# Kernel optimization log

Measured on AMD Instinct MI355X. Metric: run time of the kernel, lower is better.

## Reference

```python
import jax, jax.numpy as jnp
import numpy as np

# Static problem sizes (match input_specs): B graphs of NPG nodes each.
B = 64        # number of graphs in the batch
NPG = 1024    # nodes per graph
N = B * NPG   # total nodes
F = 64        # node feature dim
H = 128       # MLP hidden/output dim
K = 16        # knn neighbors (loop=False)


def setup_inputs() -> dict:
    key = jax.random.key(0)
    k1, k2, k3 = jax.random.split(key, 3)
    x = jax.random.normal(k1, (N, F), dtype=jnp.float32)
    batch = jnp.repeat(jnp.arange(B, dtype=jnp.int32), NPG)  # sorted graph ids
    W1 = jax.random.normal(k2, (2 * F, H), dtype=jnp.float32) / np.float32(np.sqrt(2 * F))
    b1 = jnp.zeros((H,), dtype=jnp.float32)
    W2 = jax.random.normal(k3, (H, H), dtype=jnp.float32) / np.float32(np.sqrt(H))
    b2 = jnp.zeros((H,), dtype=jnp.float32)
    return {"x": x, "batch": batch, "W1": W1, "b1": b1, "W2": W2, "b2": b2}


def _knn_edge_index(x):
    """PyG-style knn_graph (flow='source_to_target', loop=False) per graph.
    Returns (row, col) = edge_index[0], edge_index[1] where row = neighbor
    (source) node, col = center (target) node; each center has exactly K edges.
    Assumes batch ids are contiguous blocks of NPG nodes (as in setup_inputs)."""
    xb = x.reshape(B, NPG, F)
    sq = jnp.sum(xb * xb, axis=-1)                                   # [B, n]
    d = sq[:, :, None] + sq[:, None, :] - 2.0 * jnp.einsum('bnf,bmf->bnm', xb, xb)
    d = d + jnp.eye(NPG, dtype=d.dtype) * jnp.float32(1e10)          # no self loops
    _, nbr = jax.lax.top_k(-d, K)                                    # [B, n, K] local neighbor ids
    offs = (jnp.arange(B, dtype=jnp.int32) * NPG)[:, None, None]
    row = (nbr.astype(jnp.int32) + offs).reshape(-1)                 # neighbors (edge_index[0])
    centers = jnp.arange(N, dtype=jnp.int32).reshape(B, NPG, 1)
    col = jnp.broadcast_to(centers, (B, NPG, K)).reshape(-1)         # centers  (edge_index[1])
    return row, col


def reference(x, batch, W1, b1, W2, b2):
    # edge_index = knn_graph(x, k, batch, loop=False); row, col = edge_index
    row, col = _knn_edge_index(x)
    x_center = x[row]                                   # [E, F] gather
    x_neighbor = x[col]                                 # [E, F] gather
    ef = jnp.concatenate([x_center, x_neighbor - x_center], axis=-1)  # [E, 2F]
    # nn_module: Linear -> ReLU -> Linear -> ReLU
    h = jax.nn.relu(ef @ W1 + b1)
    h = jax.nn.relu(h @ W2 + b2)                        # [E, H]
    # manual scatter-mean onto row (index_add + bincount.clamp(min=1))
    node_features = jax.ops.segment_sum(h, row, num_segments=N)
    counts = jax.ops.segment_sum(jnp.ones((row.shape[0],), dtype=x.dtype), row, num_segments=N)
    counts = jnp.maximum(counts, 1.0)
    return node_features / counts[:, None]
```

## Files before the change

### kernel.cpp

```cpp
#include <hip/hip_runtime.h>

typedef __attribute__((ext_vector_type(4))) float f32x4;
typedef __attribute__((ext_vector_type(4))) unsigned int u32x4;
typedef __attribute__((ext_vector_type(8))) short s16x8;
typedef __attribute__((ext_vector_type(8))) _Float16 f16x8;

#define N_NODES 65536
#define GNPG 1024
#define FDIM 64
#define HDIM 128
#define KNN 16
#define JT 64
#define DSTR 68
#define SCAND 20
#define STKC 6
#define NEDGE (N_NODES * KNN)
#define NT (NEDGE / 64)

__global__ void prep_node_k(const float* __restrict__ x, float* __restrict__ sq,
                            double* __restrict__ sq64, _Float16* __restrict__ xf,
                            const float* __restrict__ W2, _Float16* __restrict__ w2f,
                            const float* __restrict__ W1, _Float16* __restrict__ w1cf) {
  if (blockIdx.x >= 1024) {
    int tid = threadIdx.x;
    if (blockIdx.x == 1024) {
      for (int idx = tid; idx < 8 * 4 * 64 * 8; idx += 256) {
        int j = idx & 7, l = (idx >> 3) & 63, ks = (idx >> 9) & 3, ct = idx >> 11;
        int k = 8 * (l >> 4) + j + 32 * ks, col = ct * 16 + (l & 15);
        w2f[idx] = (_Float16)W2[k * 128 + col];
      }
    } else {
      for (int idx = tid; idx < 16 * 2 * 64 * 8; idx += 256) {
        int j = idx & 7, l = (idx >> 3) & 63, ks = (idx >> 9) & 1, ct = idx >> 10;
        int k = 8 * (l >> 4) + j + 32 * ks, col = ct * 16 + (l & 15);
        float v = (col < 128) ? (W1[k * 128 + col] - W1[(k + 64) * 128 + col])
                              : W1[(k + 64) * 128 + (col - 128)];
        w1cf[idx] = (_Float16)v;
      }
    }
    return;
  }
  int t = blockIdx.x * 256 + threadIdx.x;
  int n = t >> 2, q = t & 3;
  const f32x4* xp = (const f32x4*)(x + (size_t)n * FDIM + q * 16);
  double s = 0;
  f16x8 h0, h1;
#pragma unroll
  for (int c8 = 0; c8 < 2; ++c8) {
    f32x4 a = xp[2 * c8], b = xp[2 * c8 + 1];
    f16x8 h;
#pragma unroll
    for (int e = 0; e < 4; ++e) {
      h[e] = (_Float16)a[e];
      h[4 + e] = (_Float16)b[e];
      s = fma((double)a[e], (double)a[e], s);
      s = fma((double)b[e], (double)b[e], s);
    }
    if (c8 == 0) h0 = h; else h1 = h;
  }
  *(f16x8*)(xf + (size_t)n * FDIM + q * 16) = h0;
  *(f16x8*)(xf + (size_t)n * FDIM + q * 16 + 8) = h1;
  s += __shfl_xor(s, 1);
  s += __shfl_xor(s, 2);
  if (q == 0) { sq64[n] = s; sq[n] = (float)s; }
}

__global__ __launch_bounds__(256) void prep_pq_k(const _Float16* __restrict__ xf,
                                                 const _Float16* __restrict__ w1cf,
                                                 const float* __restrict__ b1,
                                                 _Float16* __restrict__ PQ16) {
  __shared__ __attribute__((aligned(16))) _Float16 wcL[16384];
  int tid = threadIdx.x, lane = tid & 63, wave = tid >> 6;
  for (int i = tid; i < 2048; i += 256)
    *(f16x8*)(wcL + i * 8) = *(const f16x8*)(w1cf + i * 8);
  int rbase = blockIdx.x * 128 + wave * 32;
  f16x8 af[2][2];
#pragma unroll
  for (int rt = 0; rt < 2; ++rt)
#pragma unroll
    for (int ks = 0; ks < 2; ++ks) {
      size_t off = (size_t)(rbase + rt * 16 + (lane & 15)) * FDIM + (lane >> 4) * 8 + 32 * ks;
      af[rt][ks] = *(const f16x8*)(xf + off);
    }
  __syncthreads();
  f32x4 acc[2][16];
#pragma unroll
  for (int rt = 0; rt < 2; ++rt)
#pragma unroll
    for (int ct = 0; ct < 16; ++ct) acc[rt][ct] = (f32x4){0.f, 0.f, 0.f, 0.f};
#pragma unroll
  for (int ks = 0; ks < 2; ++ks)
#pragma unroll
    for (int ct = 0; ct < 16; ++ct) {
      f16x8 b = *(const f16x8*)(wcL + ((ct * 2 + ks) * 64 + lane) * 8);
#pragma unroll
      for (int rt = 0; rt < 2; ++rt)
        acc[rt][ct] = __builtin_amdgcn_mfma_f32_16x16x32_f16(af[rt][ks], b, acc[rt][ct], 0, 0, 0);
    }
  float b1r[16];
#pragma unroll
  for (int ct = 0; ct < 16; ++ct)
    b1r[ct] = (ct >= 8) ? b1[(ct - 8) * 16 + (lane & 15)] : 0.f;
#pragma unroll
  for (int rt = 0; rt < 2; ++rt)
#pragma unroll
    for (int ct = 0; ct < 16; ++ct) {
      int col = ct * 16 + (lane & 15);
#pragma unroll
      for (int r = 0; r < 4; ++r) {
        int row = rbase + rt * 16 + (lane >> 4) * 4 + r;
        PQ16[(size_t)row * 256 + col] = (_Float16)(acc[rt][ct][r] + b1r[ct]);
      }
    }
}

__global__ __launch_bounds__(256) void knn1_k(const _Float16* __restrict__ xf,
                                              const float* __restrict__ sq,
                                              unsigned short* __restrict__ candi) {
  __shared__ float sq_l[GNPG];
  __shared__ __attribute__((aligned(16))) _Float16 bfL[512 * 8];
  __shared__ __attribute__((aligned(16))) unsigned keyL[128 * DSTR];
  __shared__ __attribute__((aligned(16))) unsigned stk[STKC * 256];
  int tid = threadIdx.x, lane = tid & 63, wave = tid >> 6;
  int g = blockIdx.x >> 3;
  int rb = (blockIdx.x & 7) * 128;
  const _Float16* xfg = xf + (size_t)g * GNPG * FDIM;
  for (int i = tid; i < GNPG; i += 256) sq_l[i] = sq[g * GNPG + i] + 0.5f;
  f16x8 af[2][2];
#pragma unroll
  for (int rt = 0; rt < 2; ++rt)
#pragma unroll
    for (int ks = 0; ks < 2; ++ks) {
      size_t off = (size_t)(rb + wave * 32 + rt * 16 + (lane & 15)) * FDIM + (lane >> 4) * 8 + 32 * ks;
      af[rt][ks] = *(const f16x8*)(xfg + off);
    }
  unsigned dl[SCAND];
#pragma unroll
  for (int q = 0; q < SCAND; ++q) dl[q] = 0xFFFFFFFFu;
  int c = tid >> 1, sub = tid & 1;
  int sp = 0;
  for (int jt = 0; jt < GNPG / JT; ++jt) {
#pragma unroll
    for (int s2 = tid; s2 < 512; s2 += 256) {
      int ct = s2 >> 7, ks = (s2 >> 6) & 1, l = s2 & 63;
      size_t goff = (size_t)(jt * JT + ct * 16 + (l & 15)) * FDIM + (l >> 4) * 8 + 32 * ks;
      *(f16x8*)(bfL + s2 * 8) = *(const f16x8*)(xfg + goff);
    }
    __syncthreads();
    f32x4 acc[2][4];
#pragma unroll
    for (int rt = 0; rt < 2; ++rt)
#pragma unroll
      for (int ct = 0; ct < 4; ++ct) acc[rt][ct] = (f32x4){0.f, 0.f, 0.f, 0.f};
#pragma unroll
    for (int ks = 0; ks < 2; ++ks)
#pragma unroll
      for (int ct = 0; ct < 4; ++ct) {
        f16x8 bfr = *(const f16x8*)(bfL + ((ct * 2 + ks) * 64 + lane) * 8);
#pragma unroll
        for (int rt = 0; rt < 2; ++rt)
          acc[rt][ct] = __builtin_amdgcn_mfma_f32_16x16x32_f16(af[rt][ks], bfr, acc[rt][ct], 0, 0, 0);
      }
#pragma unroll
    for (int rt = 0; rt < 2; ++rt)
#pragma unroll
      for (int ct = 0; ct < 4; ++ct) {
        int coltl = ct * 16 + (lane & 15);
        int jlg = jt * JT + coltl;
        float sqj = sq_l[jlg];
#pragma unroll
        for (int r = 0; r < 4; ++r) {
          int row = wave * 32 + rt * 16 + (lane >> 4) * 4 + r;
          float d = sq_l[rb + row] + sqj - 2.f * acc[rt][ct][r];
          unsigned key = (__float_as_uint(d) & 0xFFFFFC00u) | (unsigned)jlg;
          if (rb + row == jlg) key = 0xFFFFFFFFu;
          keyL[row * DSTR + coltl] = key;
        }
      }
    __syncthreads();
    const unsigned* kp = keyL + c * DSTR + sub * 32;
#pragma unroll 2
    for (int i = 0; i < 8; ++i) {
      if (__any(sp > STKC - 4)) {
        while (__any(sp > 0)) {
          if (sp > 0) {
            --sp;
            unsigned k = stk[sp * 256 + tid];
            if (k < dl[SCAND - 1]) {
              dl[SCAND - 1] = k;
#pragma unroll
              for (int p = SCAND - 1; p >= 1; --p) {
                unsigned mn = min(dl[p - 1], dl[p]);
                unsigned mx = max(dl[p - 1], dl[p]);
                dl[p - 1] = mn; dl[p] = mx;
              }
            }
          }
        }
      }
      u32x4 v = *(const u32x4*)(kp + i * 4);
#pragma unroll
      for (int e = 0; e < 4; ++e) {
        stk[sp * 256 + tid] = v[e];
        sp += (v[e] < dl[SCAND - 1]) ? 1 : 0;
      }
    }
  }
  while (__any(sp > 0)) {
    if (sp > 0) {
      --sp;
      unsigned k = stk[sp * 256 + tid];
      if (k < dl[SCAND - 1]) {
        dl[SCAND - 1] = k;
#pragma unroll
        for (int p = SCAND - 1; p >= 1; --p) {
          unsigned mn = min(dl[p - 1], dl[p]);
          unsigned mx = max(dl[p - 1], dl[p]);
          dl[p - 1] = mn; dl[p] = mx;
        }
      }
    }
  }
  int nglob = g * GNPG + rb + c;
  unsigned short* ii = candi + (size_t)nglob * (2 * SCAND) + sub * SCAND;
#pragma unroll
  for (int q = 0; q < SCAND; ++q) ii[q] = (unsigned short)(dl[q] & 1023u);
}

__global__ __launch_bounds__(256) void knn2_k(const float* __restrict__ x,
                                              const double* __restrict__ sq64,
                                              const unsigned short* __restrict__ candi,
                                              int* __restrict__ nbr, int* __restrict__ counts) {
  __shared__ double md[2][128][17];
  __shared__ unsigned short mi[2][128][17];
  int tid = threadIdx.x, c_local = tid >> 1, sub = tid & 1;
  int n = blockIdx.x * 128 + c_local;
  int gbase = n & ~(GNPG - 1);
  f32x4 xi[16];
  const f32x4* xp = (const f32x4*)(x + (size_t)n * FDIM);
#pragma unroll
  for (int f = 0; f < 16; ++f) xi[f] = xp[f];
  double sq64i = sq64[n];
  double dl[KNN]; int il[KNN];
#pragma unroll
  for (int q = 0; q < KNN; ++q) { dl[q] = 1.0e300; il[q] = 0x7FFFFFFF; }
  const unsigned short* ii = candi + (size_t)n * (2 * SCAND) + sub * SCAND;
#pragma unroll 1
  for (int t = 0; t < SCAND; ++t) {
    int jl = ii[t];
    int j = gbase + jl;
    const f32x4* xj = (const f32x4*)(x + (size_t)j * FDIM);
    double t0 = 0, t1 = 0, t2 = 0, t3 = 0;
#pragma unroll
    for (int f = 0; f < 16; ++f) {
      f32x4 a = xi[f], b = xj[f];
      t0 = fma((double)a[0], (double)b[0], t0);
      t1 = fma((double)a[1], (double)b[1], t1);
      t2 = fma((double)a[2], (double)b[2], t2);
      t3 = fma((double)a[3], (double)b[3], t3);
    }
    double d = sq64i + sq64[j] - 2.0 * ((t0 + t1) + (t2 + t3));
    bool ins = (d < dl[KNN - 1]) || (d == dl[KNN - 1] && jl < il[KNN - 1]);
    if (ins) {
      dl[KNN - 1] = d; il[KNN - 1] = jl;
#pragma unroll
      for (int p = KNN - 1; p >= 1; --p) {
        double a0 = dl[p - 1], a1 = dl[p];
        int b0 = il[p - 1], b1v = il[p];
        bool cc = (a1 < a0) || (a1 == a0 && b1v < b0);
        dl[p - 1] = cc ? a1 : a0; dl[p] = cc ? a0 : a1;
        il[p - 1] = cc ? b1v : b0; il[p] = cc ? b0 : b1v;
      }
    }
  }
#pragma unroll
  for (int q = 0; q < KNN; ++q) {
    md[sub][c_local][q] = dl[q];
    mi[sub][c_local][q] = (unsigned short)il[q];
  }
  __syncthreads();
  if (sub == 0) {
    int pa = 0, pb = 0;
    for (int q = 0; q < KNN; ++q) {
      double da = md[0][c_local][pa]; int ia = mi[0][c_local][pa];
      double db = md[1][c_local][pb]; int ib = mi[1][c_local][pb];
      bool tb = (db < da) || (db == da && ib < ia);
      int iw = tb ? ib : ia;
      pa += !tb; pb += tb;
      int gidx = gbase + iw;
      nbr[(size_t)n * KNN + q] = gidx;
      atomicAdd(&counts[gidx], 1);
    }
  }
}

__global__ void scan_k(const int* __restrict__ counts, int* __restrict__ cursor) {
  __shared__ int wsum[16];
  int t = threadIdx.x;
  int base = t * 64;
  const int4* cp = (const int4*)(counts + base);
  int s = 0;
#pragma unroll
  for (int i = 0; i < 16; ++i) { int4 v = cp[i]; s += v.x + v.y + v.z + v.w; }
  int lane = t & 63, wv = t >> 6;
  int pre = s;
#pragma unroll
  for (int ofs = 1; ofs < 64; ofs <<= 1) {
    int o = __shfl_up(pre, ofs);
    if (lane >= ofs) pre += o;
  }
  if (lane == 63) wsum[wv] = pre;
  __syncthreads();
  if (t == 0) {
    int run = 0;
#pragma unroll
    for (int i = 0; i < 16; ++i) { int v = wsum[i]; wsum[i] = run; run += v; }
  }
  __syncthreads();
  int run = wsum[wv] + pre - s;
#pragma unroll
  for (int i = 0; i < 16; ++i) {
    int4 v = cp[i];
    cursor[base + 4 * i] = run; run += v.x;
    cursor[base + 4 * i + 1] = run; run += v.y;
    cursor[base + 4 * i + 2] = run; run += v.z;
    cursor[base + 4 * i + 3] = run; run += v.w;
  }
}

__global__ void scatter_k(const int* __restrict__ nbr, int* __restrict__ cursor,
                          int* __restrict__ srow, int* __restrict__ scol) {
  int e = blockIdx.x * 256 + threadIdx.x;
  int r = nbr[e], c = e >> 4;
  int pos = atomicAdd(&cursor[r], 1);
  srow[pos] = r; scol[pos] = c;
}

__global__ __launch_bounds__(256) void gemm2_k(const _Float16* __restrict__ PQ16,
                                               const int* __restrict__ srow, const int* __restrict__ scol,
                                               const _Float16* __restrict__ w2f,
                                               const float* __restrict__ b2,
                                               float* __restrict__ out) {
  __shared__ __attribute__((aligned(16))) char smem[16384];
  __shared__ int srowL[64];
  int tid = threadIdx.x, lane = tid & 63, wave = tid >> 6;
  int cg = wave & 1, eg = wave >> 1;
  f16x8 wf[4][4];
#pragma unroll
  for (int ct = 0; ct < 4; ++ct)
#pragma unroll
    for (int ks = 0; ks < 4; ++ks)
      wf[ct][ks] = *(const f16x8*)(w2f + ((((cg * 4 + ct) * 4 + ks) * 64 + lane) * 8));
  float b2r[4];
#pragma unroll
  for (int ct = 0; ct < 4; ++ct) b2r[ct] = b2[cg * 64 + ct * 16 + (lane & 15)];

  int e_in = tid >> 2, qq = tid & 3;
  f16x8 pf[8];
  int prow;
  {
    int e = blockIdx.x * 64 + e_in;
    prow = srow[e];
    int colc = scol[e];
    const f16x8* Pp = (const f16x8*)(PQ16 + (size_t)prow * 256 + qq * 32);
    const f16x8* Qp = (const f16x8*)(PQ16 + (size_t)colc * 256 + 128 + qq * 32);
#pragma unroll
    for (int i = 0; i < 4; ++i) { pf[i] = Pp[i]; pf[4 + i] = Qp[i]; }
  }
  for (int tile = blockIdx.x; tile < NT; tile += gridDim.x) {
    if (qq == 0) srowL[e_in] = prow;
#pragma unroll
    for (int i = 0; i < 4; ++i) {
      f16x8 hv;
#pragma unroll
      for (int e = 0; e < 8; ++e) {
        float sv = (float)pf[i][e] + (float)pf[4 + i][e];
        hv[e] = (_Float16)(sv > 0.f ? sv : 0.f);
      }
      int byteoff = e_in * 256 + ((2 * (qq * 32 + i * 8)) ^ ((e_in & 7) << 4));
      *(f16x8*)(smem + byteoff) = hv;
    }
    int ntile = tile + gridDim.x;
    if (ntile < NT) {
      int e = ntile * 64 + e_in;
      prow = srow[e];
      int colc = scol[e];
      const f16x8* Pp = (const f16x8*)(PQ16 + (size_t)prow * 256 + qq * 32);
      const f16x8* Qp = (const f16x8*)(PQ16 + (size_t)colc * 256 + 128 + qq * 32);
#pragma unroll
      for (int i = 0; i < 4; ++i) { pf[i] = Pp[i]; pf[4 + i] = Qp[i]; }
    }
    __syncthreads();
    f32x4 acc[2][4];
#pragma unroll
    for (int rt = 0; rt < 2; ++rt)
#pragma unroll
      for (int ct = 0; ct < 4; ++ct) acc[rt][ct] = (f32x4){0.f, 0.f, 0.f, 0.f};
#pragma unroll
    for (int rt = 0; rt < 2; ++rt) {
      int rowL = eg * 32 + rt * 16 + (lane & 15);
#pragma unroll
      for (int ks = 0; ks < 4; ++ks) {
        int byteoff = rowL * 256 + ((16 * (lane >> 4) + 64 * ks) ^ ((rowL & 7) << 4));
        f16x8 a = *(const f16x8*)(smem + byteoff);
#pragma unroll
        for (int ct = 0; ct < 4; ++ct)
          acc[rt][ct] = __builtin_amdgcn_mfma_f32_16x16x32_f16(a, wf[ct][ks], acc[rt][ct], 0, 0, 0);
      }
    }
    __syncthreads();
#pragma unroll
    for (int rt = 0; rt < 2; ++rt)
#pragma unroll
      for (int ct = 0; ct < 4; ++ct) {
        int col = cg * 64 + ct * 16 + (lane & 15);
#pragma unroll
        for (int r = 0; r < 4; ++r) {
          int row_in = eg * 32 + rt * 16 + (lane >> 4) * 4 + r;
          float v = acc[rt][ct][r] + b2r[ct];
          v = v > 0.f ? v : 0.f;
          int byteoff = row_in * 256 + ((2 * col) ^ ((row_in & 12) << 3));
          *(_Float16*)(smem + byteoff) = (_Float16)v;
        }
      }
    __syncthreads();
    {
      int col = tid & 127, estart = (tid >> 7) * 32;
      float a = 0.f;
      int prev = srowL[estart];
#pragma unroll 8
      for (int e2 = estart; e2 < estart + 32; ++e2) {
        int r2 = srowL[e2];
        if (r2 != prev) { atomicAdd(out + (size_t)prev * 128 + col, a); a = 0.f; prev = r2; }
        int byteoff = e2 * 256 + ((2 * col) ^ ((e2 & 12) << 3));
        a += (float)*(const _Float16*)(smem + byteoff);
      }
      atomicAdd(out + (size_t)prev * 128 + col, a);
    }
    __syncthreads();
  }
}

__global__ void final_k(float* __restrict__ out, const int* __restrict__ counts) {
  for (int i = blockIdx.x * 256 + threadIdx.x; i < N_NODES * 32; i += gridDim.x * 256) {
    f32x4 v = ((f32x4*)out)[i];
    int n = i >> 5;
    int c = counts[n];
    float inv = 1.0f / (float)(c > 0 ? c : 1);
    v[0] *= inv; v[1] *= inv; v[2] *= inv; v[3] *= inv;
    ((f32x4*)out)[i] = v;
  }
}

extern "C" void kernel_launch(void* const* d_in, const int* in_sizes, int n_in,
                              void* d_out, int out_size, void* d_ws, size_t ws_size,
                              hipStream_t stream) {
  const float* x = (const float*)d_in[0];
  const float* W1 = (const float*)d_in[2];
  const float* b1 = (const float*)d_in[3];
  const float* W2 = (const float*)d_in[4];
  const float* b2 = (const float*)d_in[5];
  float* out = (float*)d_out;
  char* ws = (char*)d_ws;

  _Float16* PQ16 = (_Float16*)(ws + 0);
  _Float16* xf = (_Float16*)(ws + 33554432);
  unsigned short* candi = (unsigned short*)(ws + 41943040);
  float* sq = (float*)(ws + 67108864);
  int* nbr = (int*)(ws + 67371008);
  int* counts = (int*)(ws + 71565312);
  int* cursor = (int*)(ws + 71827456);
  int* srow = (int*)(ws + 72089600);
  int* scol = (int*)(ws + 76283904);
  _Float16* w2f = (_Float16*)(ws + 80478208);
  _Float16* w1cf = (_Float16*)(ws + 80510976);
  double* sq64 = (double*)(ws + 80543744);

  hipMemsetAsync(d_out, 0, (size_t)out_size * sizeof(float), stream);
  hipMemsetAsync(counts, 0, (size_t)N_NODES * sizeof(int), stream);
  prep_node_k<<<1026, 256, 0, stream>>>(x, sq, sq64, xf, W2, w2f, W1, w1cf);
  knn1_k<<<N_NODES / 128, 256, 0, stream>>>(xf, sq, candi);
  knn2_k<<<N_NODES / 128, 256, 0, stream>>>(x, sq64, candi, nbr, counts);
  scan_k<<<1, 1024, 0, stream>>>(counts, cursor);
  scatter_k<<<NEDGE / 256, 256, 0, stream>>>(nbr, cursor, srow, scol);
  prep_pq_k<<<N_NODES / 128, 256, 0, stream>>>(xf, w1cf, b1, PQ16);
  gemm2_k<<<2048, 256, 0, stream>>>(PQ16, srow, scol, w2f, b2, out);
  final_k<<<2048, 256, 0, stream>>>(out, counts);
}
```

Measured before the change: 500.9 us.

## Split knn1 candidate scan across two column halves and merge in knn2

The approximate kNN candidate kernel now splits each graph's 1024 candidate columns into two halves handled by separate blocks, doubling the grid to raise parallelism and shorten each block's serial scan. Each half writes its sorted top-20 packed keys (distance bits plus index) to the workspace. knn2 merges the two sorted lists per thread into a top-20 before the exact fp64 re-ranking. This costs twice as much candidate storage (32-bit keys instead of 16-bit indices), an extra merge step, and the sq_l load is repeated per block.

```diff
diff --git a/kernel.cpp b/kernel.cpp
--- a/kernel.cpp
+++ b/kernel.cpp
@@ -116,14 +116,17 @@
 
 __global__ __launch_bounds__(256) void knn1_k(const _Float16* __restrict__ xf,
                                               const float* __restrict__ sq,
-                                              unsigned short* __restrict__ candi) {
+                                              unsigned* __restrict__ candk) {
   __shared__ float sq_l[GNPG];
   __shared__ __attribute__((aligned(16))) _Float16 bfL[512 * 8];
   __shared__ __attribute__((aligned(16))) unsigned keyL[128 * DSTR];
   __shared__ __attribute__((aligned(16))) unsigned stk[STKC * 256];
   int tid = threadIdx.x, lane = tid & 63, wave = tid >> 6;
-  int g = blockIdx.x >> 3;
-  int rb = (blockIdx.x & 7) * 128;
+  int g = blockIdx.x >> 4;
+  int wb = blockIdx.x & 15;
+  int rb = (wb >> 1) * 128;
+  int jh = wb & 1;
+  int jbase = jh * 512;
   const _Float16* xfg = xf + (size_t)g * GNPG * FDIM;
   for (int i = tid; i < GNPG; i += 256) sq_l[i] = sq[g * GNPG + i] + 0.5f;
   f16x8 af[2][2];
@@ -139,11 +142,11 @@
   for (int q = 0; q < SCAND; ++q) dl[q] = 0xFFFFFFFFu;
   int c = tid >> 1, sub = tid & 1;
   int sp = 0;
-  for (int jt = 0; jt < GNPG / JT; ++jt) {
+  for (int jt = 0; jt < 512 / JT; ++jt) {
 #pragma unroll
     for (int s2 = tid; s2 < 512; s2 += 256) {
       int ct = s2 >> 7, ks = (s2 >> 6) & 1, l = s2 & 63;
-      size_t goff = (size_t)(jt * JT + ct * 16 + (l & 15)) * FDIM + (l >> 4) * 8 + 32 * ks;
+      size_t goff = (size_t)(jbase + jt * JT + ct * 16 + (l & 15)) * FDIM + (l >> 4) * 8 + 32 * ks;
       *(f16x8*)(bfL + s2 * 8) = *(const f16x8*)(xfg + goff);
     }
     __syncthreads();
@@ -166,7 +169,7 @@
 #pragma unroll
       for (int ct = 0; ct < 4; ++ct) {
         int coltl = ct * 16 + (lane & 15);
-        int jlg = jt * JT + coltl;
+        int jlg = jbase + jt * JT + coltl;
         float sqj = sq_l[jlg];
 #pragma unroll
         for (int r = 0; r < 4; ++r) {
@@ -222,20 +225,33 @@
     }
   }
   int nglob = g * GNPG + rb + c;
-  unsigned short* ii = candi + (size_t)nglob * (2 * SCAND) + sub * SCAND;
-#pragma unroll
-  for (int q = 0; q < SCAND; ++q) ii[q] = (unsigned short)(dl[q] & 1023u);
+  unsigned* ok = candk + (((size_t)nglob * 2 + sub) * 2 + jh) * SCAND;
+#pragma unroll
+  for (int q = 0; q < SCAND; ++q) ok[q] = dl[q];
 }
 
 __global__ __launch_bounds__(256) void knn2_k(const float* __restrict__ x,
                                               const double* __restrict__ sq64,
-                                              const unsigned short* __restrict__ candi,
+                                              const unsigned* __restrict__ candk,
                                               int* __restrict__ nbr, int* __restrict__ counts) {
   __shared__ double md[2][128][17];
   __shared__ unsigned short mi[2][128][17];
   int tid = threadIdx.x, c_local = tid >> 1, sub = tid & 1;
   int n = blockIdx.x * 128 + c_local;
   int gbase = n & ~(GNPG - 1);
+  const unsigned* ka = candk + ((size_t)n * 2 + sub) * 2 * SCAND;
+  const unsigned* kb = ka + SCAND;
+  unsigned ml[SCAND];
+  {
+    int pa = 0, pb = 0;
+#pragma unroll
+    for (int q = 0; q < SCAND; ++q) {
+      unsigned va = ka[pa], vb = kb[pb];
+      bool tb = vb < va;
+      ml[q] = tb ? vb : va;
+      pa += !tb; pb += tb;
+    }
+  }
   f32x4 xi[16];
   const f32x4* xp = (const f32x4*)(x + (size_t)n * FDIM);
 #pragma unroll
@@ -244,10 +260,9 @@
   double dl[KNN]; int il[KNN];
 #pragma unroll
   for (int q = 0; q < KNN; ++q) { dl[q] = 1.0e300; il[q] = 0x7FFFFFFF; }
-  const unsigned short* ii = candi + (size_t)n * (2 * SCAND) + sub * SCAND;
 #pragma unroll 1
   for (int t = 0; t < SCAND; ++t) {
-    int jl = ii[t];
+    int jl = (int)(ml[t] & 1023u);
     int j = gbase + jl;
     const f32x4* xj = (const f32x4*)(x + (size_t)j * FDIM);
     double t0 = 0, t1 = 0, t2 = 0, t3 = 0;
@@ -465,7 +480,7 @@
 
   _Float16* PQ16 = (_Float16*)(ws + 0);
   _Float16* xf = (_Float16*)(ws + 33554432);
-  unsigned short* candi = (unsigned short*)(ws + 41943040);
+  unsigned* candk = (unsigned*)(ws + 41943040);
   float* sq = (float*)(ws + 67108864);
   int* nbr = (int*)(ws + 67371008);
   int* counts = (int*)(ws + 71565312);
@@ -479,8 +494,8 @@
   hipMemsetAsync(d_out, 0, (size_t)out_size * sizeof(float), stream);
   hipMemsetAsync(counts, 0, (size_t)N_NODES * sizeof(int), stream);
   prep_node_k<<<1026, 256, 0, stream>>>(x, sq, sq64, xf, W2, w2f, W1, w1cf);
-  knn1_k<<<N_NODES / 128, 256, 0, stream>>>(xf, sq, candi);
-  knn2_k<<<N_NODES / 128, 256, 0, stream>>>(x, sq64, candi, nbr, counts);
+  knn1_k<<<N_NODES / 64, 256, 0, stream>>>(xf, sq, candk);
+  knn2_k<<<N_NODES / 128, 256, 0, stream>>>(x, sq64, candk, nbr, counts);
   scan_k<<<1, 1024, 0, stream>>>(counts, cursor);
   scatter_k<<<NEDGE / 256, 256, 0, stream>>>(nbr, cursor, srow, scol);
   prep_pq_k<<<N_NODES / 128, 256, 0, stream>>>(xf, w1cf, b1, PQ16);
```

Measured after the change: 561.7 us. 12.1% more time.
